# Kernel optimization log

Hardware: AMD Instinct MI355X
Metric: run time of the kernel (lower is better)

## Reference

```python
import jax, jax.numpy as jnp
import numpy as np


def setup_inputs() -> dict:
    key = jax.random.key(0)
    k1, k2, k3, k4, k5, k6 = jax.random.split(key, 6)
    n_vars = 1000000
    n_constrs = 500000
    nnz = 20000000
    pred = jax.random.normal(k1, (n_vars,), dtype=jnp.float32)
    constr_idx = jax.random.randint(k2, (nnz,), 0, n_constrs, dtype=jnp.int32)
    var_idx = jax.random.randint(k3, (nnz,), 0, n_vars, dtype=jnp.int32)
    coeff = jax.random.normal(k4, (nnz,), dtype=jnp.float32)
    constr_rhs = jax.random.normal(k5, (n_constrs,), dtype=jnp.float32)
    constr_sense = jax.random.randint(k6, (n_constrs,), 1, 4, dtype=jnp.int32)  # 1=<=, 2=>=, 3===
    return {
        "pred": pred,
        "constr_idx": constr_idx,
        "var_idx": var_idx,
        "coeff": coeff,
        "constr_rhs": constr_rhs,
        "constr_sense": constr_sense,
        "n_vars": n_vars,
        "n_constrs": n_constrs,
    }


def reference(pred, constr_idx, var_idx, coeff, constr_rhs, constr_sense, n_vars, n_constrs):
    # probs = sigmoid(pred); ax[i] = sum over nnz entries of coeff * probs[var_idx]
    probs = jax.nn.sigmoid(pred)
    contrib = coeff * probs[var_idx]                      # [nnz]
    ax = jax.ops.segment_sum(contrib, constr_idx, num_segments=n_constrs)  # [n_constrs]
    le = jax.nn.relu(ax - constr_rhs)      # sense == 1 (<=)
    ge = jax.nn.relu(constr_rhs - ax)      # sense == 2 (>=)
    eq = jnp.abs(ax - constr_rhs)          # sense == 3 (==)
    violations = jnp.where(constr_sense == 1, le,
                  jnp.where(constr_sense == 2, ge,
                   jnp.where(constr_sense == 3, eq, jnp.zeros_like(ax))))
    return violations.mean()  # reduction='mean'
```

## Files before the change

kernel.cpp:

```cpp
#include <hip/hip_runtime.h>
#include <math.h>

#define R_LOG2 13
#define R_BKT  8192
#define SLICE  16
#define MAXNB  64
#define RECS_PER_BLK 4096


__global__ void init_fast(const float* __restrict__ pred,
                          float* __restrict__ probs,
                          unsigned* __restrict__ cursor,
                          float* __restrict__ out,
                          int n_vars, int nb) {
    int i = blockIdx.x * blockDim.x + threadIdx.x;
    if (i < n_vars) probs[i] = 1.0f / (1.0f + expf(-pred[i]));
    if (i < nb) cursor[i] = 0;
    if (i == 0) out[0] = 0.0f;
}

__global__ __launch_bounds__(256) void partition_kernel(
        const int* __restrict__ cidx, const int* __restrict__ vidx,
        const float* __restrict__ coeff, const float* __restrict__ probs,
        unsigned* __restrict__ cursor, unsigned* __restrict__ recs,
        int nnz4, int nb, unsigned cap) {
    __shared__ unsigned hist[256];
    __shared__ unsigned scan[256];
    __shared__ unsigned lcur[256];
    __shared__ unsigned bstart[MAXNB + 1];
    __shared__ unsigned gbase[MAXNB];
    __shared__ unsigned sorted[RECS_PER_BLK];

    const int tid = threadIdx.x;
    const int sub = tid >> 6;

    unsigned rw[16];
    unsigned bk[16];
    bool     gv[4];
    #pragma unroll
    for (int g = 0; g < 4; ++g) {
        unsigned v = blockIdx.x * 1024u + g * 256u + (unsigned)tid;
        gv[g] = v < (unsigned)nnz4;
        if (gv[g]) {
            int4   c4 = ((const int4*)cidx)[v];
            int4   v4 = ((const int4*)vidx)[v];
            float4 w4 = ((const float4*)coeff)[v];
            int   cc[4] = {c4.x, c4.y, c4.z, c4.w};
            float vv[4] = {w4.x * probs[v4.x], w4.y * probs[v4.y],
                           w4.z * probs[v4.z], w4.w * probs[v4.w]};
            #pragma unroll
            for (int j = 0; j < 4; ++j) {
                int k = g * 4 + j;
                unsigned bits = __builtin_bit_cast(unsigned, vv[j]);
                bits += 0x7FFFu + ((bits >> 16) & 1u);
                rw[k] = ((unsigned)(cc[j] & (R_BKT - 1)) << 16) | (bits >> 16);
                bk[k] = (unsigned)cc[j] >> R_LOG2;
            }
        }
    }

    hist[tid] = 0;
    __syncthreads();
    #pragma unroll
    for (int g = 0; g < 4; ++g) if (gv[g]) {
        #pragma unroll
        for (int j = 0; j < 4; ++j)
            atomicAdd(&hist[bk[g * 4 + j] * 4 + sub], 1u);
    }
    __syncthreads();

    scan[tid] = hist[tid];
    __syncthreads();
    #pragma unroll
    for (int d = 1; d < 256; d <<= 1) {
        unsigned t = (tid >= d) ? scan[tid - d] : 0u;
        __syncthreads();
        if (tid >= d) scan[tid] += t;
        __syncthreads();
    }

    lcur[tid] = scan[tid] - hist[tid];
    if (tid < nb) bstart[tid] = scan[tid * 4] - hist[tid * 4];
    if (tid == 0) bstart[nb] = scan[255];
    __syncthreads();
    if (tid < nb) {
        unsigned cnt = bstart[tid + 1] - bstart[tid];
        gbase[tid] = cnt ? atomicAdd(&cursor[tid], cnt) : 0u;
    }
    __syncthreads();

    #pragma unroll
    for (int g = 0; g < 4; ++g) if (gv[g]) {
        #pragma unroll
        for (int j = 0; j < 4; ++j) {
            int k = g * 4 + j;
            unsigned lpos = atomicAdd(&lcur[bk[k] * 4 + sub], 1u);
            sorted[lpos] = rw[k];
        }
    }
    __syncthreads();

    unsigned total = bstart[nb];
    for (unsigned p = tid; p < total; p += 256u) {
        unsigned lo = 0, hi = (unsigned)nb - 1;
        while (lo < hi) {
            unsigned mid = (lo + hi + 1) >> 1;
            if (bstart[mid] <= p) lo = mid; else hi = mid - 1;
        }
        unsigned pos = gbase[lo] + (p - bstart[lo]);
        if (pos < cap) recs[(size_t)lo * cap + pos] = sorted[p];
    }
}

__global__ __launch_bounds__(256) void accum_kernel(
        const unsigned* __restrict__ recs, const unsigned* __restrict__ cursor,
        float* __restrict__ partial, int n_constrs, unsigned cap) {
    __shared__ float acc[R_BKT];
    const int b = blockIdx.x / SLICE;
    const int s = blockIdx.x % SLICE;
    for (int j = threadIdx.x; j < R_BKT; j += blockDim.x) acc[j] = 0.0f;
    __syncthreads();

    unsigned cnt = cursor[b];
    if (cnt > cap) cnt = cap;
    unsigned start = (unsigned)(((unsigned long long)cnt * s) / SLICE);
    unsigned end   = (unsigned)(((unsigned long long)cnt * (s + 1)) / SLICE);
    const unsigned* base = recs + (size_t)b * cap;
    for (unsigned i = start + threadIdx.x; i < end; i += blockDim.x) {
        unsigned r = base[i];
        float v = __builtin_bit_cast(float, (r & 0xFFFFu) << 16);
        unsafeAtomicAdd(&acc[r >> 16], v);
    }
    __syncthreads();

    const int gb = b * R_BKT;
    float* dst = partial + (size_t)s * n_constrs;
    for (int j = threadIdx.x * 4; j < R_BKT; j += blockDim.x * 4) {
        int g = gb + j;
        if (g < n_constrs) {
            float4 v4 = make_float4(acc[j], acc[j+1], acc[j+2], acc[j+3]);
            *(float4*)(dst + g) = v4;
        }
    }
}

__global__ void reduce_fast(const float* __restrict__ partial,
                            const float* __restrict__ rhs,
                            const int* __restrict__ sense,
                            float* __restrict__ out,
                            int n_constrs, float inv_n) {
    int i = blockIdx.x * blockDim.x + threadIdx.x;
    float v = 0.0f;
    if (i < n_constrs) {
        float a = 0.0f;
        #pragma unroll
        for (int s = 0; s < SLICE; ++s)
            a += partial[(size_t)s * n_constrs + i];
        float d = a - rhs[i];
        int sn = sense[i];
        v = (sn == 1) ? fmaxf(d, 0.0f)
          : (sn == 2) ? fmaxf(-d, 0.0f)
          : (sn == 3) ? fabsf(d)
          : 0.0f;
    }
    #pragma unroll
    for (int off = 32; off > 0; off >>= 1)
        v += __shfl_down(v, off, 64);
    __shared__ float wsum[4];
    int lane = threadIdx.x & 63;
    int wid  = threadIdx.x >> 6;
    if (lane == 0) wsum[wid] = v;
    __syncthreads();
    if (threadIdx.x == 0)
        atomicAdd(out, (wsum[0] + wsum[1] + wsum[2] + wsum[3]) * inv_n);
}


__global__ void init_kernel(const float* __restrict__ pred,
                            float* __restrict__ probs,
                            float* __restrict__ ax,
                            float* __restrict__ out,
                            int n_vars, int n_constrs) {
    int i = blockIdx.x * blockDim.x + threadIdx.x;
    if (i < n_vars) probs[i] = 1.0f / (1.0f + expf(-pred[i]));
    if (i < n_constrs) ax[i] = 0.0f;
    if (i == 0) out[0] = 0.0f;
}

__global__ void scatter_kernel(const int* __restrict__ cidx,
                               const int* __restrict__ vidx,
                               const float* __restrict__ coeff,
                               const float* __restrict__ probs,
                               float* __restrict__ ax,
                               int nnz) {
    int i = blockIdx.x * blockDim.x + threadIdx.x;
    long long base = (long long)i * 4;
    if (base + 3 < (long long)nnz) {
        int4   c = ((const int4*)cidx)[i];
        int4   v = ((const int4*)vidx)[i];
        float4 w = ((const float4*)coeff)[i];
        unsafeAtomicAdd(&ax[c.x], w.x * probs[v.x]);
        unsafeAtomicAdd(&ax[c.y], w.y * probs[v.y]);
        unsafeAtomicAdd(&ax[c.z], w.z * probs[v.z]);
        unsafeAtomicAdd(&ax[c.w], w.w * probs[v.w]);
    } else if (base < (long long)nnz) {
        for (long long k = base; k < (long long)nnz; ++k)
            unsafeAtomicAdd(&ax[cidx[k]], coeff[k] * probs[vidx[k]]);
    }
}

__global__ void reduce_kernel(const float* __restrict__ ax,
                              const float* __restrict__ rhs,
                              const int* __restrict__ sense,
                              float* __restrict__ out,
                              int n_constrs, float inv_n) {
    int i = blockIdx.x * blockDim.x + threadIdx.x;
    float v = 0.0f;
    if (i < n_constrs) {
        float d = ax[i] - rhs[i];
        int s = sense[i];
        v = (s == 1) ? fmaxf(d, 0.0f)
          : (s == 2) ? fmaxf(-d, 0.0f)
          : (s == 3) ? fabsf(d)
          : 0.0f;
    }
    #pragma unroll
    for (int off = 32; off > 0; off >>= 1)
        v += __shfl_down(v, off, 64);
    __shared__ float wsum[4];
    int lane = threadIdx.x & 63;
    int wid  = threadIdx.x >> 6;
    if (lane == 0) wsum[wid] = v;
    __syncthreads();
    if (threadIdx.x == 0)
        atomicAdd(out, (wsum[0] + wsum[1] + wsum[2] + wsum[3]) * inv_n);
}


static inline size_t align16(size_t x) { return (x + 15) & ~(size_t)15; }

extern "C" void kernel_launch(void* const* d_in, const int* in_sizes, int n_in,
                              void* d_out, int out_size, void* d_ws, size_t ws_size,
                              hipStream_t stream) {
    const float* pred  = (const float*)d_in[0];
    const int*   cidx  = (const int*)d_in[1];
    const int*   vidx  = (const int*)d_in[2];
    const float* coeff = (const float*)d_in[3];
    const float* rhs   = (const float*)d_in[4];
    const int*   sense = (const int*)d_in[5];

    const int n_vars    = in_sizes[0];
    const int nnz       = in_sizes[1];
    const int n_constrs = in_sizes[4];
    const int B = 256;
    const float inv_n = 1.0f / (float)n_constrs;

    const int nb = (n_constrs + R_BKT - 1) / R_BKT;
    unsigned cap = (unsigned)(((double)nnz * R_BKT / (double)n_constrs) * 1.0625) + 1024;

    size_t off_probs  = 0;
    size_t off_cursor = align16(off_probs + (size_t)n_vars * 4);
    size_t off_recs   = align16(off_cursor + (size_t)nb * 4);
    size_t off_part   = align16(off_recs + (size_t)nb * cap * 4);
    size_t need_fast  = off_part + (size_t)SLICE * n_constrs * 4;

    bool fast = (ws_size >= need_fast) && (nb <= MAXNB) && ((nnz & 3) == 0);

    if (fast) {
        float*    probs   = (float*)((char*)d_ws + off_probs);
        unsigned* cursor  = (unsigned*)((char*)d_ws + off_cursor);
        unsigned* recs    = (unsigned*)((char*)d_ws + off_recs);
        float*    partial = (float*)((char*)d_ws + off_part);
        float*    out     = (float*)d_out;

        int init_n = n_vars > nb ? n_vars : nb;
        init_fast<<<(init_n + B - 1) / B, B, 0, stream>>>(
            pred, probs, cursor, out, n_vars, nb);

        int nnz4 = nnz >> 2;
        int nblk1 = (nnz4 + 1023) / 1024;
        partition_kernel<<<nblk1, B, 0, stream>>>(
            cidx, vidx, coeff, probs, cursor, recs, nnz4, nb, cap);

        accum_kernel<<<nb * SLICE, B, 0, stream>>>(
            recs, cursor, partial, n_constrs, cap);

        reduce_fast<<<(n_constrs + B - 1) / B, B, 0, stream>>>(
            partial, rhs, sense, out, n_constrs, inv_n);
    } else {
        float* probs = (float*)d_ws;
        float* ax    = probs + n_vars;
        float* out   = (float*)d_out;

        int init_n = n_vars > n_constrs ? n_vars : n_constrs;
        init_kernel<<<(init_n + B - 1) / B, B, 0, stream>>>(
            pred, probs, ax, out, n_vars, n_constrs);

        int n_vec_threads = (nnz + 3) / 4;
        scatter_kernel<<<(n_vec_threads + B - 1) / B, B, 0, stream>>>(
            cidx, vidx, coeff, probs, ax, nnz);

        reduce_kernel<<<(n_constrs + B - 1) / B, B, 0, stream>>>(
            ax, rhs, sense, out, n_constrs, inv_n);
    }
}
```

Measured before the change: 512.2 us.

## Partition per wavefront without block barriers; vectorize accumulation record loads

The partition kernel now lets each 64-lane wavefront bucket its own 1024 records. It uses a wave-level shuffle scan and per-wave global cursor atomics, which removes the block-wide __syncthreads chain and the binary search for the destination bucket. Each sorted record's bucket id is stored in a byte array in shared memory. The accumulate kernel reads records as uint4 with a scalar tail, and cap is rounded to a multiple of 4 for alignment. Global atomics on the cursors rise fourfold, and the scatter runs become smaller, so writes may coalesce less well.

New measurement: 700.5 us. 1.37x slower.

```diff
diff --git a/kernel.cpp b/kernel.cpp
--- a/kernel.cpp
+++ b/kernel.cpp
@@ -5,7 +5,7 @@
 #define R_BKT  8192
 #define SLICE  16
 #define MAXNB  64
-#define RECS_PER_BLK 4096
+#define WAVE_RECS 1024
 
 
 __global__ void init_fast(const float* __restrict__ pred,
@@ -24,22 +24,25 @@
         const float* __restrict__ coeff, const float* __restrict__ probs,
         unsigned* __restrict__ cursor, unsigned* __restrict__ recs,
         int nnz4, int nb, unsigned cap) {
-    __shared__ unsigned hist[256];
-    __shared__ unsigned scan[256];
-    __shared__ unsigned lcur[256];
-    __shared__ unsigned bstart[MAXNB + 1];
-    __shared__ unsigned gbase[MAXNB];
-    __shared__ unsigned sorted[RECS_PER_BLK];
-
-    const int tid = threadIdx.x;
-    const int sub = tid >> 6;
+    __shared__ unsigned      sorted[4][WAVE_RECS];
+    __shared__ unsigned char sortedB[4][WAVE_RECS];
+    __shared__ unsigned      lcur[4][MAXNB];
+    __shared__ unsigned      bst[4][MAXNB + 1];
+    __shared__ unsigned      gbs[4][MAXNB];
+
+    const int tid  = threadIdx.x;
+    const int w    = tid >> 6;
+    const int lane = tid & 63;
+
+    if (lane < MAXNB) lcur[w][lane] = 0;
 
     unsigned rw[16];
     unsigned bk[16];
     bool     gv[4];
+    const unsigned vbase = blockIdx.x * 1024u + (unsigned)w * 256u;
     #pragma unroll
     for (int g = 0; g < 4; ++g) {
-        unsigned v = blockIdx.x * 1024u + g * 256u + (unsigned)tid;
+        unsigned v = vbase + (unsigned)g * 64u + (unsigned)lane;
         gv[g] = v < (unsigned)nnz4;
         if (gv[g]) {
             int4   c4 = ((const int4*)cidx)[v];
@@ -59,56 +62,46 @@
         }
     }
 
-    hist[tid] = 0;
-    __syncthreads();
     #pragma unroll
     for (int g = 0; g < 4; ++g) if (gv[g]) {
         #pragma unroll
         for (int j = 0; j < 4; ++j)
-            atomicAdd(&hist[bk[g * 4 + j] * 4 + sub], 1u);
-    }
-    __syncthreads();
-
-    scan[tid] = hist[tid];
-    __syncthreads();
-    #pragma unroll
-    for (int d = 1; d < 256; d <<= 1) {
-        unsigned t = (tid >= d) ? scan[tid - d] : 0u;
-        __syncthreads();
-        if (tid >= d) scan[tid] += t;
-        __syncthreads();
-    }
-
-    lcur[tid] = scan[tid] - hist[tid];
-    if (tid < nb) bstart[tid] = scan[tid * 4] - hist[tid * 4];
-    if (tid == 0) bstart[nb] = scan[255];
-    __syncthreads();
-    if (tid < nb) {
-        unsigned cnt = bstart[tid + 1] - bstart[tid];
-        gbase[tid] = cnt ? atomicAdd(&cursor[tid], cnt) : 0u;
-    }
-    __syncthreads();
+            atomicAdd(&lcur[w][bk[g * 4 + j]], 1u);
+    }
+
+    unsigned cnt = (lane < nb) ? lcur[w][lane] : 0u;
+    unsigned sc = cnt;
+    #pragma unroll
+    for (int d = 1; d < 64; d <<= 1) {
+        unsigned t = __shfl_up(sc, d, 64);
+        if (lane >= d) sc += t;
+    }
+    unsigned excl  = sc - cnt;
+    unsigned total = __shfl(sc, nb - 1, 64);
+
+    if (lane < nb) {
+        bst[w][lane]  = excl;
+        gbs[w][lane]  = cnt ? atomicAdd(&cursor[lane], cnt) : 0u;
+        lcur[w][lane] = excl;
+    }
+    if (lane == 0) bst[w][nb] = total;
 
     #pragma unroll
     for (int g = 0; g < 4; ++g) if (gv[g]) {
         #pragma unroll
         for (int j = 0; j < 4; ++j) {
             int k = g * 4 + j;
-            unsigned lpos = atomicAdd(&lcur[bk[k] * 4 + sub], 1u);
-            sorted[lpos] = rw[k];
+            unsigned pos = atomicAdd(&lcur[w][bk[k]], 1u);
+            sorted[w][pos]  = rw[k];
+            sortedB[w][pos] = (unsigned char)bk[k];
         }
     }
-    __syncthreads();
-
-    unsigned total = bstart[nb];
-    for (unsigned p = tid; p < total; p += 256u) {
-        unsigned lo = 0, hi = (unsigned)nb - 1;
-        while (lo < hi) {
-            unsigned mid = (lo + hi + 1) >> 1;
-            if (bstart[mid] <= p) lo = mid; else hi = mid - 1;
-        }
-        unsigned pos = gbase[lo] + (p - bstart[lo]);
-        if (pos < cap) recs[(size_t)lo * cap + pos] = sorted[p];
+
+    for (unsigned p = (unsigned)lane; p < total; p += 64u) {
+        unsigned r = sorted[w][p];
+        unsigned b = sortedB[w][p];
+        unsigned pos = gbs[w][b] + (p - bst[w][b]);
+        if (pos < cap) recs[(size_t)b * cap + pos] = r;
     }
 }
 
@@ -118,18 +111,31 @@
     __shared__ float acc[R_BKT];
     const int b = blockIdx.x / SLICE;
     const int s = blockIdx.x % SLICE;
-    for (int j = threadIdx.x; j < R_BKT; j += blockDim.x) acc[j] = 0.0f;
+    for (int j = threadIdx.x * 4; j < R_BKT; j += blockDim.x * 4)
+        *(float4*)(acc + j) = make_float4(0.f, 0.f, 0.f, 0.f);
     __syncthreads();
 
     unsigned cnt = cursor[b];
     if (cnt > cap) cnt = cap;
-    unsigned start = (unsigned)(((unsigned long long)cnt * s) / SLICE);
-    unsigned end   = (unsigned)(((unsigned long long)cnt * (s + 1)) / SLICE);
     const unsigned* base = recs + (size_t)b * cap;
-    for (unsigned i = start + threadIdx.x; i < end; i += blockDim.x) {
-        unsigned r = base[i];
-        float v = __builtin_bit_cast(float, (r & 0xFFFFu) << 16);
-        unsafeAtomicAdd(&acc[r >> 16], v);
+
+    unsigned c4 = cnt >> 2;
+    unsigned s4 = (unsigned)(((unsigned long long)c4 * s) / SLICE);
+    unsigned e4 = (unsigned)(((unsigned long long)c4 * (s + 1)) / SLICE);
+    const uint4* b4 = (const uint4*)base;
+    #pragma unroll 2
+    for (unsigned i = s4 + threadIdx.x; i < e4; i += blockDim.x) {
+        uint4 r = b4[i];
+        unsafeAtomicAdd(&acc[r.x >> 16], __builtin_bit_cast(float, (r.x & 0xFFFFu) << 16));
+        unsafeAtomicAdd(&acc[r.y >> 16], __builtin_bit_cast(float, (r.y & 0xFFFFu) << 16));
+        unsafeAtomicAdd(&acc[r.z >> 16], __builtin_bit_cast(float, (r.z & 0xFFFFu) << 16));
+        unsafeAtomicAdd(&acc[r.w >> 16], __builtin_bit_cast(float, (r.w & 0xFFFFu) << 16));
+    }
+    if (s == SLICE - 1) {
+        for (unsigned i = (c4 << 2) + threadIdx.x; i < cnt; i += blockDim.x) {
+            unsigned r = base[i];
+            unsafeAtomicAdd(&acc[r >> 16], __builtin_bit_cast(float, (r & 0xFFFFu) << 16));
+        }
     }
     __syncthreads();
 
@@ -137,10 +143,8 @@
     float* dst = partial + (size_t)s * n_constrs;
     for (int j = threadIdx.x * 4; j < R_BKT; j += blockDim.x * 4) {
         int g = gb + j;
-        if (g < n_constrs) {
-            float4 v4 = make_float4(acc[j], acc[j+1], acc[j+2], acc[j+3]);
-            *(float4*)(dst + g) = v4;
-        }
+        if (g < n_constrs)
+            *(float4*)(dst + g) = make_float4(acc[j], acc[j+1], acc[j+2], acc[j+3]);
     }
 }
 
@@ -257,6 +261,7 @@
 
     const int nb = (n_constrs + R_BKT - 1) / R_BKT;
     unsigned cap = (unsigned)(((double)nnz * R_BKT / (double)n_constrs) * 1.0625) + 1024;
+    cap = (cap + 3u) & ~3u;
 
     size_t off_probs  = 0;
     size_t off_cursor = align16(off_probs + (size_t)n_vars * 4);
```
